# Optimization experiments

Hardware: AMD Instinct MI355X
Metric: run time of the kernel (lower is better)

The kernel has to match this reference:

```python
import jax, jax.numpy as jnp
import numpy as np

B, S, D = 16, 512, 1024
H, HD = 16, 64          # head, head_dim; attn_dim = H*HD = D
FF = 4096               # linear_dim
EPS = 1e-6              # flax LayerNorm default epsilon


def _layernorm(x, scale):
    # flax LayerNorm(use_bias=False, use_scale=True)
    m = jnp.mean(x, axis=-1, keepdims=True)
    v = jnp.mean(jnp.square(x - m), axis=-1, keepdims=True)
    return (x - m) * jax.lax.rsqrt(v + EPS) * scale


def _attention(c, wq, wk, wv, wo):
    b, s, _ = c.shape
    q = (c @ wq).reshape(b, s, H, HD)
    k = (c @ wk).reshape(b, s, H, HD)
    v = (c @ wv).reshape(b, s, H, HD)
    score = jnp.einsum('bihd,bjhd->bijh', q, k) / jnp.sqrt(jnp.asarray(HD, c.dtype))
    score = jax.nn.softmax(score, axis=2)
    out = jnp.einsum('bijh,bjhd->bihd', score, v).reshape(b, s, H * HD)
    return out @ wo


def _mlp(x, w1, b1, w2, b2):
    return jax.nn.gelu(x @ w1 + b1) @ w2 + b2


def setup_inputs() -> dict:
    key = jax.random.key(0)
    ks = jax.random.split(key, 8)
    sd = 1.0 / np.sqrt(D)
    sf = 1.0 / np.sqrt(FF)
    return {
        'x': jax.random.normal(ks[0], (B, S, D), jnp.float32),
        'wq': jax.random.normal(ks[1], (D, D), jnp.float32) * sd,
        'wk': jax.random.normal(ks[2], (D, D), jnp.float32) * sd,
        'wv': jax.random.normal(ks[3], (D, D), jnp.float32) * sd,
        'wo': jax.random.normal(ks[4], (D, D), jnp.float32) * sd,
        'ln1_scale': jnp.ones((D,), jnp.float32),
        'ln2_scale': jnp.ones((D,), jnp.float32),
        'w1': jax.random.normal(ks[5], (D, FF), jnp.float32) * sd,
        'b1': jnp.zeros((FF,), jnp.float32),
        'w2': jax.random.normal(ks[6], (FF, D), jnp.float32) * sf,
        'b2': jnp.zeros((D,), jnp.float32),
    }


def reference(x, wq, wk, wv, wo, ln1_scale, ln2_scale, w1, b1, w2, b2):
    # inference mode: dropout / stochastic depth are identity
    c = _layernorm(x, ln1_scale)
    a = _attention(c, wq, wk, wv, wo)
    x = x + a           # x + dropout(attn(c,c))
    x = x + a           # x + attn(c,c)  (source adds attention output twice)
    x = x + _mlp(_layernorm(x, ln2_scale), w1, b1, w2, b2)
    x = x + _mlp(_layernorm(x, ln2_scale), w1, b1, w2, b2)
    return x
```

## Files before the change

kernel.cpp:

```cpp
#include <hip/hip_runtime.h>
#include <hip/hip_bf16.h>

typedef _Float16 f16;
typedef _Float16 f16x8 __attribute__((ext_vector_type(8)));
typedef _Float16 f16x4 __attribute__((ext_vector_type(4)));
typedef float    f32x4 __attribute__((ext_vector_type(4)));

#define MFMA16x16x32(a, b, c) __builtin_amdgcn_mfma_f32_16x16x32_f16(a, b, c, 0, 0, 0)

__device__ inline float gelu_f(float x) {
    float z = 0.79788456080286535588f * (x + 0.044715f * x * x * x);
    float e = __expf(2.0f * z);
    float t = 1.0f - 2.0f / (e + 1.0f);
    return 0.5f * x * (1.0f + t);
}

__global__ __launch_bounds__(256) void transpose_wt(const float* __restrict__ in,
                                                    f16* __restrict__ out,
                                                    int K, int N) {
    __shared__ float tile[32][33];
    int n0 = blockIdx.x * 32, k0 = blockIdx.y * 32;
    int tx = threadIdx.x & 31, ty = threadIdx.x >> 5;
#pragma unroll
    for (int i = 0; i < 32; i += 8)
        tile[ty + i][tx] = in[(size_t)(k0 + ty + i) * N + n0 + tx];
    __syncthreads();
#pragma unroll
    for (int i = 0; i < 32; i += 8)
        out[(size_t)(n0 + ty + i) * K + k0 + tx] = (f16)tile[tx][ty + i];
}

__global__ __launch_bounds__(256) void ln_f16(const float* __restrict__ x,
                                              const float* __restrict__ g,
                                              f16* __restrict__ out) {
    int row = blockIdx.x, t = threadIdx.x;
    float4 v = ((const float4*)(x + (size_t)row * 1024))[t];
    float s  = v.x + v.y + v.z + v.w;
    float s2 = v.x * v.x + v.y * v.y + v.z * v.z + v.w * v.w;
#pragma unroll
    for (int off = 1; off < 64; off <<= 1) {
        s  += __shfl_xor(s, off);
        s2 += __shfl_xor(s2, off);
    }
    __shared__ float red[8];
    int w = t >> 6, lane = t & 63;
    if (lane == 0) { red[w] = s; red[4 + w] = s2; }
    __syncthreads();
    s  = red[0] + red[1] + red[2] + red[3];
    s2 = red[4] + red[5] + red[6] + red[7];
    float mean = s * (1.0f / 1024.0f);
    float var  = s2 * (1.0f / 1024.0f) - mean * mean;
    float r = rsqrtf(var + 1e-6f);
    float4 gv = ((const float4*)g)[t];
    f16x4 ov;
    ov[0] = (f16)((v.x - mean) * r * gv.x);
    ov[1] = (f16)((v.y - mean) * r * gv.y);
    ov[2] = (f16)((v.z - mean) * r * gv.z);
    ov[3] = (f16)((v.w - mean) * r * gv.w);
    *(f16x4*)(out + (size_t)row * 1024 + t * 4) = ov;
}

template <int EPI>
__global__ __launch_bounds__(256) void gemm_f16(
    const f16* __restrict__ A, const f16* __restrict__ Bt,
    const float* __restrict__ bias, const float* __restrict__ resid,
    float* __restrict__ outF, f16* __restrict__ outH,
    int M, int N, int K, float rscale) {
    __shared__ __align__(16) f16 As[128 * 64];
    __shared__ __align__(16) f16 Bs[128 * 64];

    const int t = threadIdx.x, lane = t & 63, w = t >> 6;
    const int wm = w >> 1, wn = w & 1;
    const int l15 = lane & 15, lg = lane >> 4, l7 = lane & 7;
    const int m0 = blockIdx.y * 128, n0 = blockIdx.x * 128;

    f32x4 acc[4][4] = {};

    int rows[4], slots[4];
#pragma unroll
    for (int i = 0; i < 4; ++i) {
        int c = i * 256 + t;
        rows[i] = c >> 3;
        slots[i] = c & 7;
    }

    f16x8 va[4], vb[4];
#pragma unroll
    for (int i = 0; i < 4; ++i) {
        va[i] = *(const f16x8*)(A + (size_t)(m0 + rows[i]) * K + slots[i] * 8);
        vb[i] = *(const f16x8*)(Bt + (size_t)(n0 + rows[i]) * K + slots[i] * 8);
    }

    for (int kt = 0; kt < K; kt += 64) {
        __syncthreads();
#pragma unroll
        for (int i = 0; i < 4; ++i) {
            int off = rows[i] * 128 + ((slots[i] ^ (rows[i] & 7)) * 16);
            *(f16x8*)((char*)As + off) = va[i];
            *(f16x8*)((char*)Bs + off) = vb[i];
        }
        if (kt + 64 < K) {
#pragma unroll
            for (int i = 0; i < 4; ++i) {
                va[i] = *(const f16x8*)(A + (size_t)(m0 + rows[i]) * K + kt + 64 + slots[i] * 8);
                vb[i] = *(const f16x8*)(Bt + (size_t)(n0 + rows[i]) * K + kt + 64 + slots[i] * 8);
            }
        }
        __syncthreads();

        f16x8 af[2][4], bf[2][4];
#pragma unroll
        for (int xt = 0; xt < 4; ++xt) {
            int ra = wm * 64 + xt * 16 + l15;
            int rb = wn * 64 + xt * 16 + l15;
#pragma unroll
            for (int kk = 0; kk < 2; ++kk) {
                af[kk][xt] = *(const f16x8*)((char*)As + ra * 128 + (((kk * 4 + lg) ^ l7) * 16));
                bf[kk][xt] = *(const f16x8*)((char*)Bs + rb * 128 + (((kk * 4 + lg) ^ l7) * 16));
            }
        }
#pragma unroll
        for (int kk = 0; kk < 2; ++kk)
#pragma unroll
            for (int mt = 0; mt < 4; ++mt)
#pragma unroll
                for (int nt = 0; nt < 4; ++nt)
                    acc[mt][nt] = MFMA16x16x32(af[kk][mt], bf[kk][nt], acc[mt][nt]);
    }

#pragma unroll
    for (int mt = 0; mt < 4; ++mt) {
#pragma unroll
        for (int nt = 0; nt < 4; ++nt) {
            int colL = n0 + wn * 64 + nt * 16 + l15;
#pragma unroll
            for (int j = 0; j < 4; ++j) {
                int rowL = m0 + wm * 64 + mt * 16 + lg * 4 + j;
                size_t idx = (size_t)rowL * N + colL;
                float vv = acc[mt][nt][j];
                if constexpr (EPI == 0) {
                    outH[idx] = (f16)vv;
                } else if constexpr (EPI == 1) {
                    vv += bias[colL];
                    outH[idx] = (f16)gelu_f(vv);
                } else if constexpr (EPI == 2) {
                    outF[idx] = resid[idx] + rscale * vv;
                } else {
                    outF[idx] = resid[idx] + vv + bias[colL];
                }
            }
        }
    }
}

__global__ __launch_bounds__(256) void attn_f16(const f16* __restrict__ q,
                                                const f16* __restrict__ k,
                                                const f16* __restrict__ v,
                                                f16* __restrict__ o) {
    __shared__ __align__(16) f16 Ks[512 * 64];
    __shared__ __align__(16) f16 Vt[64 * 512];
    __shared__ __align__(16) f16 Ps[4][16 * 32];

    const int t = threadIdx.x, lane = t & 63, w = t >> 6;
    const int l15 = lane & 15, lg = lane >> 4;
    const int bh = blockIdx.x, b = bh >> 4, h = bh & 15;
    const f16* kg = k + (size_t)(b * 512) * 1024 + h * 64;
    const f16* vg = v + (size_t)(b * 512) * 1024 + h * 64;
    const f16* qg = q + (size_t)(b * 512) * 1024 + h * 64;

#pragma unroll
    for (int i = 0; i < 16; ++i) {
        int c = i * 256 + t, r = c >> 3, s = c & 7;
        f16x8 val = *(const f16x8*)(kg + (size_t)r * 1024 + s * 8);
        *(f16x8*)((char*)Ks + r * 128 + ((s ^ (r & 7)) * 16)) = val;
    }
#pragma unroll
    for (int i = 0; i < 16; ++i) {
        int c = i * 256 + t, r = c >> 3, s = c & 7;
        f16x8 val = *(const f16x8*)(vg + (size_t)r * 1024 + s * 8);
#pragma unroll
        for (int dd = 0; dd < 8; ++dd) {
            int d = s * 8 + dd;
            *(f16*)((char*)Vt + d * 1024 + ((r * 2) ^ ((d & 7) << 4))) = val[dd];
        }
    }
    __syncthreads();

    for (int it = 0; it < 8; ++it) {
        int q0 = it * 64 + w * 16;
        f16x8 aq[2];
#pragma unroll
        for (int kk = 0; kk < 2; ++kk)
            aq[kk] = *(const f16x8*)(qg + (size_t)(q0 + l15) * 1024 + kk * 32 + lg * 8);

        f32x4 sc[32] = {};
#pragma unroll
        for (int jt = 0; jt < 32; ++jt) {
#pragma unroll
            for (int kk = 0; kk < 2; ++kk) {
                int row = jt * 16 + l15;
                f16x8 bk = *(const f16x8*)((char*)Ks + row * 128 + (((kk * 4 + lg) ^ (l15 & 7)) * 16));
                sc[jt] = MFMA16x16x32(aq[kk], bk, sc[jt]);
            }
        }

        float inv_sum[4];
#pragma unroll
        for (int r4 = 0; r4 < 4; ++r4) {
            float m = sc[0][r4];
#pragma unroll
            for (int jt = 1; jt < 32; ++jt) m = fmaxf(m, sc[jt][r4]);
#pragma unroll
            for (int off = 1; off < 16; off <<= 1) m = fmaxf(m, __shfl_xor(m, off));
            float sum = 0.0f;
#pragma unroll
            for (int jt = 0; jt < 32; ++jt) {
                float p = __expf((sc[jt][r4] - m) * 0.125f);
                sc[jt][r4] = p;
                sum += p;
            }
#pragma unroll
            for (int off = 1; off < 16; off <<= 1) sum += __shfl_xor(sum, off);
            inv_sum[r4] = 1.0f / sum;
        }

        f32x4 oa[4] = {};
        f16* myPs = &Ps[w][0];
#pragma unroll
        for (int u = 0; u < 16; ++u) {
#pragma unroll
            for (int half = 0; half < 2; ++half) {
                int jt = 2 * u + half;
#pragma unroll
                for (int r4 = 0; r4 < 4; ++r4) {
                    int row = lg * 4 + r4;
                    int colb = (half * 16 + l15) * 2;
                    *(f16*)((char*)myPs + row * 64 + (colb ^ (((row >> 1) & 3) << 4))) =
                        (f16)sc[jt][r4];
                }
            }
            f16x8 pa = *(const f16x8*)((char*)myPs + l15 * 64 + ((lg ^ ((l15 >> 1) & 3)) * 16));
#pragma unroll
            for (int ct = 0; ct < 4; ++ct) {
                int vrow = ct * 16 + l15;
                f16x8 bv = *(const f16x8*)((char*)Vt + vrow * 1024 + (((u * 4 + lg) ^ (vrow & 7)) * 16));
                oa[ct] = MFMA16x16x32(pa, bv, oa[ct]);
            }
        }

#pragma unroll
        for (int ct = 0; ct < 4; ++ct)
#pragma unroll
            for (int j = 0; j < 4; ++j) {
                int row = q0 + lg * 4 + j;
                int col = h * 64 + ct * 16 + l15;
                o[(size_t)(b * 512 + row) * 1024 + col] = (f16)(oa[ct][j] * inv_sum[j]);
            }
    }
}

extern "C" void kernel_launch(void* const* d_in, const int* in_sizes, int n_in,
                              void* d_out, int out_size, void* d_ws, size_t ws_size,
                              hipStream_t stream) {
    (void)in_sizes; (void)n_in; (void)out_size; (void)ws_size;
    const float* x   = (const float*)d_in[0];
    const float* wq  = (const float*)d_in[1];
    const float* wk  = (const float*)d_in[2];
    const float* wv  = (const float*)d_in[3];
    const float* wo  = (const float*)d_in[4];
    const float* ln1 = (const float*)d_in[5];
    const float* ln2 = (const float*)d_in[6];
    const float* w1  = (const float*)d_in[7];
    const float* b1  = (const float*)d_in[8];
    const float* w2  = (const float*)d_in[9];
    const float* b2  = (const float*)d_in[10];
    float* outF = (float*)d_out;

    char* ws = (char*)d_ws;
    size_t o = 0;
    f16* WqT = (f16*)(ws + o); o += (size_t)1024 * 1024 * 2;
    f16* WkT = (f16*)(ws + o); o += (size_t)1024 * 1024 * 2;
    f16* WvT = (f16*)(ws + o); o += (size_t)1024 * 1024 * 2;
    f16* WoT = (f16*)(ws + o); o += (size_t)1024 * 1024 * 2;
    f16* W1T = (f16*)(ws + o); o += (size_t)4096 * 1024 * 2;
    f16* W2T = (f16*)(ws + o); o += (size_t)1024 * 4096 * 2;
    f16* cb  = (f16*)(ws + o); o += (size_t)8192 * 1024 * 2;
    f16* qb  = (f16*)(ws + o); o += (size_t)8192 * 1024 * 2;
    f16* kb  = (f16*)(ws + o); o += (size_t)8192 * 1024 * 2;
    f16* vb  = (f16*)(ws + o); o += (size_t)8192 * 1024 * 2;
    f16* hb  = (f16*)(ws + o); o += (size_t)8192 * 4096 * 2;
    float* x2 = (float*)(ws + o); o += (size_t)8192 * 1024 * 4;

    dim3 tb(256);
    transpose_wt<<<dim3(32, 32), tb, 0, stream>>>(wq, WqT, 1024, 1024);
    transpose_wt<<<dim3(32, 32), tb, 0, stream>>>(wk, WkT, 1024, 1024);
    transpose_wt<<<dim3(32, 32), tb, 0, stream>>>(wv, WvT, 1024, 1024);
    transpose_wt<<<dim3(32, 32), tb, 0, stream>>>(wo, WoT, 1024, 1024);
    transpose_wt<<<dim3(128, 32), tb, 0, stream>>>(w1, W1T, 1024, 4096);
    transpose_wt<<<dim3(32, 128), tb, 0, stream>>>(w2, W2T, 4096, 1024);

    ln_f16<<<8192, tb, 0, stream>>>(x, ln1, cb);
    gemm_f16<0><<<dim3(8, 64), tb, 0, stream>>>(cb, WqT, nullptr, nullptr, nullptr, qb, 8192, 1024, 1024, 0.f);
    gemm_f16<0><<<dim3(8, 64), tb, 0, stream>>>(cb, WkT, nullptr, nullptr, nullptr, kb, 8192, 1024, 1024, 0.f);
    gemm_f16<0><<<dim3(8, 64), tb, 0, stream>>>(cb, WvT, nullptr, nullptr, nullptr, vb, 8192, 1024, 1024, 0.f);
    attn_f16<<<dim3(256), tb, 0, stream>>>(qb, kb, vb, cb);
    gemm_f16<2><<<dim3(8, 64), tb, 0, stream>>>(cb, WoT, nullptr, x, outF, nullptr, 8192, 1024, 1024, 2.0f);
    ln_f16<<<8192, tb, 0, stream>>>(outF, ln2, cb);
    gemm_f16<1><<<dim3(32, 64), tb, 0, stream>>>(cb, W1T, b1, nullptr, nullptr, hb, 8192, 4096, 1024, 0.f);
    gemm_f16<3><<<dim3(8, 64), tb, 0, stream>>>(hb, W2T, b2, outF, x2, nullptr, 8192, 1024, 4096, 1.0f);
    ln_f16<<<8192, tb, 0, stream>>>(x2, ln2, cb);
    gemm_f16<1><<<dim3(32, 64), tb, 0, stream>>>(cb, W1T, b1, nullptr, nullptr, hb, 8192, 4096, 1024, 0.f);
    gemm_f16<3><<<dim3(8, 64), tb, 0, stream>>>(hb, W2T, b2, x2, outF, nullptr, 8192, 1024, 4096, 1.0f);
}
```

Before: 682.4 us.

## Replace GEMM with 8-wave 256-wide tiled kernel using direct global-to-LDS loads and fused QKV

Replaces the 128x128 register-staged GEMM with a 512-thread kernel computing 256x256 or 128x256 tiles. It double-buffers LDS filled by global_load_lds, interleaves fragment loads, barriers and MFMA quarters with setprio, and swizzles block order for L2 locality. The three Q/K/V projections are merged into one GEMM over a concatenated transposed weight, and attention reads from the packed QKV buffer with stride 3072. It targets low MFMA utilisation and load latency in the old GEMM, at the cost of reliance on hand-placed waitcnt counts and larger LDS and register use per block.

```diff
diff --git a/kernel.cpp b/kernel.cpp
--- a/kernel.cpp
+++ b/kernel.cpp
@@ -7,6 +7,13 @@
 typedef float    f32x4 __attribute__((ext_vector_type(4)));
 
 #define MFMA16x16x32(a, b, c) __builtin_amdgcn_mfma_f32_16x16x32_f16(a, b, c, 0, 0, 0)
+
+typedef __attribute__((address_space(1))) const void GASV;
+typedef __attribute__((address_space(3))) void LASV;
+
+#define WAIT_LGKM0 asm volatile("s_waitcnt lgkmcnt(0)" ::: "memory")
+#define WAIT_VM2   asm volatile("s_waitcnt vmcnt(2)" ::: "memory")
+#define WAIT_VM4   asm volatile("s_waitcnt vmcnt(4)" ::: "memory")
 
 __device__ inline float gelu_f(float x) {
     float z = 0.79788456080286535588f * (x + 0.044715f * x * x * x);
@@ -60,84 +67,153 @@
     *(f16x4*)(out + (size_t)row * 1024 + t * 4) = ov;
 }
 
-template <int EPI>
-__global__ __launch_bounds__(256) void gemm_f16(
+template <int BM, int EPI>
+__global__ __launch_bounds__(512, 2) void gemm8(
     const f16* __restrict__ A, const f16* __restrict__ Bt,
     const float* __restrict__ bias, const float* __restrict__ resid,
     float* __restrict__ outF, f16* __restrict__ outH,
     int M, int N, int K, float rscale) {
-    __shared__ __align__(16) f16 As[128 * 64];
-    __shared__ __align__(16) f16 Bs[128 * 64];
-
-    const int t = threadIdx.x, lane = t & 63, w = t >> 6;
-    const int wm = w >> 1, wn = w & 1;
-    const int l15 = lane & 15, lg = lane >> 4, l7 = lane & 7;
-    const int m0 = blockIdx.y * 128, n0 = blockIdx.x * 128;
-
-    f32x4 acc[4][4] = {};
-
-    int rows[4], slots[4];
-#pragma unroll
-    for (int i = 0; i < 4; ++i) {
-        int c = i * 256 + t;
-        rows[i] = c >> 3;
-        slots[i] = c & 7;
-    }
-
-    f16x8 va[4], vb[4];
-#pragma unroll
-    for (int i = 0; i < 4; ++i) {
-        va[i] = *(const f16x8*)(A + (size_t)(m0 + rows[i]) * K + slots[i] * 8);
-        vb[i] = *(const f16x8*)(Bt + (size_t)(n0 + rows[i]) * K + slots[i] * 8);
-    }
-
-    for (int kt = 0; kt < K; kt += 64) {
-        __syncthreads();
-#pragma unroll
-        for (int i = 0; i < 4; ++i) {
-            int off = rows[i] * 128 + ((slots[i] ^ (rows[i] & 7)) * 16);
-            *(f16x8*)((char*)As + off) = va[i];
-            *(f16x8*)((char*)Bs + off) = vb[i];
-        }
-        if (kt + 64 < K) {
-#pragma unroll
-            for (int i = 0; i < 4; ++i) {
-                va[i] = *(const f16x8*)(A + (size_t)(m0 + rows[i]) * K + kt + 64 + slots[i] * 8);
-                vb[i] = *(const f16x8*)(Bt + (size_t)(n0 + rows[i]) * K + kt + 64 + slots[i] * 8);
-            }
-        }
-        __syncthreads();
-
-        f16x8 af[2][4], bf[2][4];
-#pragma unroll
-        for (int xt = 0; xt < 4; ++xt) {
-            int ra = wm * 64 + xt * 16 + l15;
-            int rb = wn * 64 + xt * 16 + l15;
-#pragma unroll
-            for (int kk = 0; kk < 2; ++kk) {
-                af[kk][xt] = *(const f16x8*)((char*)As + ra * 128 + (((kk * 4 + lg) ^ l7) * 16));
-                bf[kk][xt] = *(const f16x8*)((char*)Bs + rb * 128 + (((kk * 4 + lg) ^ l7) * 16));
-            }
-        }
-#pragma unroll
-        for (int kk = 0; kk < 2; ++kk)
-#pragma unroll
-            for (int mt = 0; mt < 4; ++mt)
-#pragma unroll
-                for (int nt = 0; nt < 4; ++nt)
-                    acc[mt][nt] = MFMA16x16x32(af[kk][mt], bf[kk][nt], acc[mt][nt]);
-    }
-
-#pragma unroll
-    for (int mt = 0; mt < 4; ++mt) {
-#pragma unroll
-        for (int nt = 0; nt < 4; ++nt) {
-            int colL = n0 + wn * 64 + nt * 16 + l15;
+    static_assert(BM == 256 || BM == 128, "BM");
+    constexpr int AH   = BM / 128;
+    constexpr int MREP = BM / 32;
+    constexpr int MH   = MREP / 2;
+
+    __shared__ __align__(16) f16 lds[2][AH + 2][128 * 64];
+
+    const int t512 = threadIdx.x;
+    const int lane = t512 & 63, w = t512 >> 6;
+    const int l15 = lane & 15, lg = lane >> 4;
+    const int wr = w >> 2, wc = w & 3;
+
+    const int nwg = gridDim.x;
+    const int bid = blockIdx.x;
+    const int swz = (bid & 7) * (nwg >> 3) + (bid >> 3);
+    const int nbn = N >> 8;
+    const int bm = swz / nbn, bn = swz % nbn;
+    const int m0 = bm * BM, n0 = bn * 256;
+    const int NT = K >> 6;
+
+    const int ahalf = (BM == 256) ? wr : 0;
+    const int arow0 = (BM == 256) ? 0 : wr * 64;
+    const int bhalf = AH + (wc >> 1);
+    const int brow0 = (wc & 1) * 64;
+
+    auto stage = [&](int kt, int half) {
+        if (kt >= NT) return;
+        f16* dst0 = &lds[kt & 1][half][0];
+        const bool isA = (half < AH);
+        const f16* Mat = isA ? A : Bt;
+        const int rb = isA ? (m0 + half * 128) : (n0 + (half - AH) * 128);
+#pragma unroll
+        for (int u = 0; u < 2; ++u) {
+            int c = u * 512 + t512;
+            int cs = c ^ (((c >> 5) & 1) << 1);
+            const f16* src = Mat + (size_t)(rb + (cs >> 3)) * K + kt * 64 + (cs & 7) * 8;
+            __builtin_amdgcn_global_load_lds((GASV*)src, (LASV*)(dst0 + c * 8), 16, 0, 0);
+        }
+    };
+    auto ldfrag = [&](int cur, int half, int rh, int s) -> f16x8 {
+        int ps = s ^ (((rh >> 2) & 1) << 1);
+        return *(const f16x8*)(&lds[cur][half][0] + rh * 64 + ps * 8);
+    };
+
+    f32x4 acc[MREP][4] = {};
+    f16x8 faL[2][MH], faH[2][MH], fb[2][4];
+
+#pragma unroll
+    for (int h = 0; h < AH + 2; ++h) stage(0, h);
+#pragma unroll
+    for (int h = 0; h < AH; ++h) stage(1, h);
+    if (BM == 256) { WAIT_VM4; } else { WAIT_VM2; }
+    __builtin_amdgcn_s_barrier();
+
+    for (int t = 0; t < NT; ++t) {
+        const int cur = t & 1;
+#pragma unroll
+        for (int ks = 0; ks < 2; ++ks) {
+#pragma unroll
+            for (int i = 0; i < MH; ++i) {
+                int rh = arow0 + i * 16 + l15;
+                faL[ks][i] = ldfrag(cur, ahalf, rh, ks * 4 + lg);
+            }
 #pragma unroll
             for (int j = 0; j < 4; ++j) {
-                int rowL = m0 + wm * 64 + mt * 16 + lg * 4 + j;
+                int rh = brow0 + j * 16 + l15;
+                fb[ks][j] = ldfrag(cur, bhalf, rh, ks * 4 + lg);
+            }
+        }
+        stage(t + 1, AH + 0);
+        __builtin_amdgcn_s_barrier();
+        WAIT_LGKM0;
+        __builtin_amdgcn_s_setprio(1);
+#pragma unroll
+        for (int i = 0; i < MH; ++i)
+#pragma unroll
+            for (int j = 0; j < 2; ++j)
+#pragma unroll
+                for (int ks = 0; ks < 2; ++ks)
+                    acc[i][j] = MFMA16x16x32(faL[ks][i], fb[ks][j], acc[i][j]);
+        __builtin_amdgcn_s_setprio(0);
+        __builtin_amdgcn_s_barrier();
+        stage(t + 1, AH + 1);
+        __builtin_amdgcn_s_barrier();
+        WAIT_LGKM0;
+        __builtin_amdgcn_s_setprio(1);
+#pragma unroll
+        for (int i = 0; i < MH; ++i)
+#pragma unroll
+            for (int j = 0; j < 2; ++j)
+#pragma unroll
+                for (int ks = 0; ks < 2; ++ks)
+                    acc[i][2 + j] = MFMA16x16x32(faL[ks][i], fb[ks][2 + j], acc[i][2 + j]);
+        __builtin_amdgcn_s_setprio(0);
+        __builtin_amdgcn_s_barrier();
+#pragma unroll
+        for (int ks = 0; ks < 2; ++ks)
+#pragma unroll
+            for (int i = 0; i < MH; ++i) {
+                int rh = arow0 + (MH + i) * 16 + l15;
+                faH[ks][i] = ldfrag(cur, ahalf, rh, ks * 4 + lg);
+            }
+        __builtin_amdgcn_s_barrier();
+        WAIT_LGKM0;
+        __builtin_amdgcn_s_setprio(1);
+#pragma unroll
+        for (int i = 0; i < MH; ++i)
+#pragma unroll
+            for (int j = 0; j < 2; ++j)
+#pragma unroll
+                for (int ks = 0; ks < 2; ++ks)
+                    acc[MH + i][j] = MFMA16x16x32(faH[ks][i], fb[ks][j], acc[MH + i][j]);
+        __builtin_amdgcn_s_setprio(0);
+        __builtin_amdgcn_s_barrier();
+#pragma unroll
+        for (int h = 0; h < AH; ++h) stage(t + 2, h);
+        __builtin_amdgcn_s_barrier();
+        WAIT_LGKM0;
+        __builtin_amdgcn_s_setprio(1);
+#pragma unroll
+        for (int i = 0; i < MH; ++i)
+#pragma unroll
+            for (int j = 0; j < 2; ++j)
+#pragma unroll
+                for (int ks = 0; ks < 2; ++ks)
+                    acc[MH + i][2 + j] = MFMA16x16x32(faH[ks][i], fb[ks][2 + j], acc[MH + i][2 + j]);
+        __builtin_amdgcn_s_setprio(0);
+        if (BM == 256) { WAIT_VM4; } else { WAIT_VM2; }
+        __builtin_amdgcn_s_barrier();
+    }
+
+#pragma unroll
+    for (int mi = 0; mi < MREP; ++mi) {
+#pragma unroll
+        for (int ni = 0; ni < 4; ++ni) {
+            int colL = n0 + wc * 64 + ni * 16 + l15;
+#pragma unroll
+            for (int j = 0; j < 4; ++j) {
+                int rowL = m0 + ((BM == 256) ? wr * 128 : wr * 64) + mi * 16 + lg * 4 + j;
                 size_t idx = (size_t)rowL * N + colL;
-                float vv = acc[mt][nt][j];
+                float vv = acc[mi][ni][j];
                 if constexpr (EPI == 0) {
                     outH[idx] = (f16)vv;
                 } else if constexpr (EPI == 1) {
@@ -153,10 +229,8 @@
     }
 }
 
-__global__ __launch_bounds__(256) void attn_f16(const f16* __restrict__ q,
-                                                const f16* __restrict__ k,
-                                                const f16* __restrict__ v,
-                                                f16* __restrict__ o) {
+__global__ __launch_bounds__(256) void attn_f16(const f16* __restrict__ qkv,
+                                                int ld, f16* __restrict__ o) {
     __shared__ __align__(16) f16 Ks[512 * 64];
     __shared__ __align__(16) f16 Vt[64 * 512];
     __shared__ __align__(16) f16 Ps[4][16 * 32];
@@ -164,20 +238,20 @@
     const int t = threadIdx.x, lane = t & 63, w = t >> 6;
     const int l15 = lane & 15, lg = lane >> 4;
     const int bh = blockIdx.x, b = bh >> 4, h = bh & 15;
-    const f16* kg = k + (size_t)(b * 512) * 1024 + h * 64;
-    const f16* vg = v + (size_t)(b * 512) * 1024 + h * 64;
-    const f16* qg = q + (size_t)(b * 512) * 1024 + h * 64;
+    const f16* qg = qkv + (size_t)(b * 512) * ld + h * 64;
+    const f16* kg = qg + 1024;
+    const f16* vg = qg + 2048;
 
 #pragma unroll
     for (int i = 0; i < 16; ++i) {
         int c = i * 256 + t, r = c >> 3, s = c & 7;
-        f16x8 val = *(const f16x8*)(kg + (size_t)r * 1024 + s * 8);
+        f16x8 val = *(const f16x8*)(kg + (size_t)r * ld + s * 8);
         *(f16x8*)((char*)Ks + r * 128 + ((s ^ (r & 7)) * 16)) = val;
     }
 #pragma unroll
     for (int i = 0; i < 16; ++i) {
         int c = i * 256 + t, r = c >> 3, s = c & 7;
-        f16x8 val = *(const f16x8*)(vg + (size_t)r * 1024 + s * 8);
+        f16x8 val = *(const f16x8*)(vg + (size_t)r * ld + s * 8);
 #pragma unroll
         for (int dd = 0; dd < 8; ++dd) {
             int d = s * 8 + dd;
@@ -191,7 +265,7 @@
         f16x8 aq[2];
 #pragma unroll
         for (int kk = 0; kk < 2; ++kk)
-            aq[kk] = *(const f16x8*)(qg + (size_t)(q0 + l15) * 1024 + kk * 32 + lg * 8);
+            aq[kk] = *(const f16x8*)(qg + (size_t)(q0 + l15) * ld + kk * 32 + lg * 8);
 
         f32x4 sc[32] = {};
 #pragma unroll
@@ -278,37 +352,37 @@
 
     char* ws = (char*)d_ws;
     size_t o = 0;
-    f16* WqT = (f16*)(ws + o); o += (size_t)1024 * 1024 * 2;
-    f16* WkT = (f16*)(ws + o); o += (size_t)1024 * 1024 * 2;
-    f16* WvT = (f16*)(ws + o); o += (size_t)1024 * 1024 * 2;
-    f16* WoT = (f16*)(ws + o); o += (size_t)1024 * 1024 * 2;
-    f16* W1T = (f16*)(ws + o); o += (size_t)4096 * 1024 * 2;
-    f16* W2T = (f16*)(ws + o); o += (size_t)1024 * 4096 * 2;
-    f16* cb  = (f16*)(ws + o); o += (size_t)8192 * 1024 * 2;
-    f16* qb  = (f16*)(ws + o); o += (size_t)8192 * 1024 * 2;
-    f16* kb  = (f16*)(ws + o); o += (size_t)8192 * 1024 * 2;
-    f16* vb  = (f16*)(ws + o); o += (size_t)8192 * 1024 * 2;
-    f16* hb  = (f16*)(ws + o); o += (size_t)8192 * 4096 * 2;
-    float* x2 = (float*)(ws + o); o += (size_t)8192 * 1024 * 4;
-
-    dim3 tb(256);
-    transpose_wt<<<dim3(32, 32), tb, 0, stream>>>(wq, WqT, 1024, 1024);
-    transpose_wt<<<dim3(32, 32), tb, 0, stream>>>(wk, WkT, 1024, 1024);
-    transpose_wt<<<dim3(32, 32), tb, 0, stream>>>(wv, WvT, 1024, 1024);
+    f16* WqkvT = (f16*)(ws + o); o += (size_t)3072 * 1024 * 2;
+    f16* WoT   = (f16*)(ws + o); o += (size_t)1024 * 1024 * 2;
+    f16* W1T   = (f16*)(ws + o); o += (size_t)4096 * 1024 * 2;
+    f16* W2T   = (f16*)(ws + o); o += (size_t)1024 * 4096 * 2;
+    f16* cb    = (f16*)(ws + o); o += (size_t)8192 * 1024 * 2;
+    f16* qkvb  = (f16*)(ws + o); o += (size_t)8192 * 3072 * 2;
+    f16* hb    = (f16*)(ws + o); o += (size_t)8192 * 4096 * 2;
+    float* x2  = (float*)(ws + o); o += (size_t)8192 * 1024 * 4;
+
+    dim3 tb(256), tg(512);
+    transpose_wt<<<dim3(32, 32), tb, 0, stream>>>(wq, WqkvT, 1024, 1024);
+    transpose_wt<<<dim3(32, 32), tb, 0, stream>>>(wk, WqkvT + (size_t)1024 * 1024, 1024, 1024);
+    transpose_wt<<<dim3(32, 32), tb, 0, stream>>>(wv, WqkvT + (size_t)2048 * 1024, 1024, 1024);
     transpose_wt<<<dim3(32, 32), tb, 0, stream>>>(wo, WoT, 1024, 1024);
     transpose_wt<<<dim3(128, 32), tb, 0, stream>>>(w1, W1T, 1024, 4096);
     transpose_wt<<<dim3(32, 128), tb, 0, stream>>>(w2, W2T, 4096, 1024);
 
     ln_f16<<<8192, tb, 0, stream>>>(x, ln1, cb);
-    gemm_f16<0><<<dim3(8, 64), tb, 0, stream>>>(cb, WqT, nullptr, nullptr, nullptr, qb, 8192, 1024, 1024, 0.f);
-    gemm_f16<0><<<dim3(8, 64), tb, 0, stream>>>(cb, WkT, nullptr, nullptr, nullptr, kb, 8192, 1024, 1024, 0.f);
-    gemm_f16<0><<<dim3(8, 64), tb, 0, stream>>>(cb, WvT, nullptr, nullptr, nullptr, vb, 8192, 1024, 1024, 0.f);
-    attn_f16<<<dim3(256), tb, 0, stream>>>(qb, kb, vb, cb);
-    gemm_f16<2><<<dim3(8, 64), tb, 0, stream>>>(cb, WoT, nullptr, x, outF, nullptr, 8192, 1024, 1024, 2.0f);
+    gemm8<256, 0><<<384, tg, 0, stream>>>(cb, WqkvT, nullptr, nullptr, nullptr, qkvb,
+                                          8192, 3072, 1024, 0.f);
+    attn_f16<<<256, tb, 0, stream>>>(qkvb, 3072, cb);
+    gemm8<128, 2><<<256, tg, 0, stream>>>(cb, WoT, nullptr, x, outF, nullptr,
+                                          8192, 1024, 1024, 2.0f);
     ln_f16<<<8192, tb, 0, stream>>>(outF, ln2, cb);
-    gemm_f16<1><<<dim3(32, 64), tb, 0, stream>>>(cb, W1T, b1, nullptr, nullptr, hb, 8192, 4096, 1024, 0.f);
-    gemm_f16<3><<<dim3(8, 64), tb, 0, stream>>>(hb, W2T, b2, outF, x2, nullptr, 8192, 1024, 4096, 1.0f);
+    gemm8<256, 1><<<512, tg, 0, stream>>>(cb, W1T, b1, nullptr, nullptr, hb,
+                                          8192, 4096, 1024, 0.f);
+    gemm8<128, 3><<<256, tg, 0, stream>>>(hb, W2T, b2, outF, x2, nullptr,
+                                          8192, 1024, 4096, 1.0f);
     ln_f16<<<8192, tb, 0, stream>>>(x2, ln2, cb);
-    gemm_f16<1><<<dim3(32, 64), tb, 0, stream>>>(cb, W1T, b1, nullptr, nullptr, hb, 8192, 4096, 1024, 0.f);
-    gemm_f16<3><<<dim3(8, 64), tb, 0, stream>>>(hb, W2T, b2, x2, outF, nullptr, 8192, 1024, 4096, 1.0f);
-}
+    gemm8<256, 1><<<512, tg, 0, stream>>>(cb, W1T, b1, nullptr, nullptr, hb,
+                                          8192, 4096, 1024, 0.f);
+    gemm8<128, 3><<<256, tg, 0, stream>>>(hb, W2T, b2, x2, outF, nullptr,
+                                          8192, 1024, 4096, 1.0f);
+}
```

Result: faster. 666.1 us (-2.4%).
